# Kernel optimization log

Measured on AMD Instinct MI355X. Metric: run time of the kernel, lower is better.

The kernel has to match this reference:

```python
import jax, jax.numpy as jnp
import numpy as np

NUM_HEADS = 32
NUM_KV_HEADS = 8
HEAD_DIM = 128
SEQ = 2048
MASK_BLOCK = 128  # diffusion-LM denoising block size


def setup_inputs() -> dict:
    key = jax.random.key(0)
    kq, kk, kv = jax.random.split(key, 3)
    q = jax.random.normal(kq, (SEQ, NUM_HEADS * HEAD_DIM), dtype=jnp.float32)
    k = jax.random.normal(kk, (SEQ, NUM_KV_HEADS * HEAD_DIM), dtype=jnp.float32)
    v = jax.random.normal(kv, (SEQ, NUM_KV_HEADS * HEAD_DIM), dtype=jnp.float32)
    # block-causal mask at MASK_BLOCK granularity: token_q attends to token_kv
    # iff block(token_kv) <= block(token_q). Every row has >=1 True entry.
    blk = jnp.arange(SEQ) // MASK_BLOCK
    block_mask = blk[None, :] <= blk[:, None]  # [S, S] bool
    return {"q": q, "k": k, "v": v, "block_mask": block_mask}


def reference(q, k, v, block_mask):
    S = q.shape[0]
    scale = 1.0 / np.sqrt(HEAD_DIM).astype(np.float32)  # flex_attention default scale
    qh = q.reshape(S, NUM_HEADS, HEAD_DIM)       # [S, Hq, D]
    kh = k.reshape(S, NUM_KV_HEADS, HEAD_DIM)    # [S, Hkv, D]
    vh = v.reshape(S, NUM_KV_HEADS, HEAD_DIM)
    # GQA: repeat each kv head over its query-head group
    group = NUM_HEADS // NUM_KV_HEADS
    kh = jnp.repeat(kh, group, axis=1)           # [S, Hq, D]
    vh = jnp.repeat(vh, group, axis=1)
    scores = jnp.einsum('qhd,khd->hqk', qh, kh) * scale  # [Hq, S, S]
    neg_inf = jnp.finfo(scores.dtype).min
    scores = jnp.where(block_mask[None, :, :], scores, neg_inf)
    probs = jax.nn.softmax(scores, axis=-1)
    o = jnp.einsum('hqk,khd->qhd', probs, vh)    # [S, Hq, D]
    return o.reshape(S, NUM_HEADS * HEAD_DIM)
```

## Files before the change

kernel.cpp:

```cpp
#include <hip/hip_runtime.h>
#include <hip/hip_bf16.h>

#define SEQL  2048
#define NHQ   32
#define NHKV  8
#define HD    128

typedef __attribute__((ext_vector_type(4))) float          f32x4;
typedef __attribute__((ext_vector_type(8))) short          bf16x8;
typedef __attribute__((ext_vector_type(4))) unsigned short u16x4;
typedef __attribute__((ext_vector_type(8))) unsigned short u16x8;

__device__ __forceinline__ unsigned short f2bf(float f) {
  union { float f; unsigned u; } v; v.f = f;
  unsigned u = v.u;
  return (unsigned short)((u + 0x7fffu + ((u >> 16) & 1u)) >> 16);
}

__device__ __forceinline__ unsigned cvtpk_bf16(float lo, float hi) {
  unsigned r;
  asm("v_cvt_pk_bf16_f32 %0, %1, %2" : "=v"(r) : "v"(lo), "v"(hi));
  return r;
}

__device__ __forceinline__ void gload16(const void* g, void* l) {
  __builtin_amdgcn_global_load_lds(
      (const __attribute__((address_space(1))) unsigned int*)g,
      (__attribute__((address_space(3))) unsigned int*)l, 16, 0, 0);
}

__global__ __launch_bounds__(256) void prep_k(const float* __restrict__ k,
                                              unsigned short* __restrict__ kws) {
  int t = blockIdx.x * 256 + threadIdx.x;
  int s   = t >> 7;
  int col = (t & 127) << 3;
  int hkv = col >> 7;
  int d0  = col & 127;
  const float* src = k + (size_t)s * (NHKV * HD) + col;
  f32x4 a = *(const f32x4*)src;
  f32x4 b = *(const f32x4*)(src + 4);
  u16x8 r;
  r[0] = f2bf(a[0]); r[1] = f2bf(a[1]); r[2] = f2bf(a[2]); r[3] = f2bf(a[3]);
  r[4] = f2bf(b[0]); r[5] = f2bf(b[1]); r[6] = f2bf(b[2]); r[7] = f2bf(b[3]);
  int tile = s >> 6, rr = s & 63;
  int idx = (rr * 128 + d0) ^ ((rr & 7) << 3);
  *(u16x8*)(kws + (((size_t)(hkv * 32 + tile)) << 13) + idx) = r;
}

__global__ __launch_bounds__(256) void prep_v(const float* __restrict__ v,
                                              unsigned short* __restrict__ vws) {
  int t = blockIdx.x * 256 + threadIdx.x;
  int d    = t & 127;
  int hkv  = (t >> 7) & 7;
  int rest = t >> 10;
  int tile = rest >> 3;
  int g    = (rest >> 2) & 1;
  int lhi  = rest & 3;
  int s0   = tile * 64 + g * 32 + lhi * 4;
  const float* src = v + (size_t)s0 * (NHKV * HD) + hkv * HD + d;
  u16x8 r;
  #pragma unroll
  for (int j = 0; j < 8; ++j) {
    int soff = ((j >> 2) << 4) + (j & 3);
    r[j] = f2bf(src[(size_t)soff * (NHKV * HD)]);
  }
  int idx = (d * 64 + g * 32 + lhi * 8) ^ ((d & 7) << 3);
  *(u16x8*)(vws + (((size_t)(hkv * 32 + tile)) << 13) + idx) = r;
}

__global__ __launch_bounds__(256, 2) void attn_fwd11(
    const float* __restrict__ q,
    const unsigned short* __restrict__ kws,
    const unsigned short* __restrict__ vws,
    float* __restrict__ out)
{
  __shared__ unsigned short Kb[2][8192];
  __shared__ unsigned short Vb[2][8192];

  const int tid  = threadIdx.x;
  const int lane = tid & 63;
  const int wv   = tid >> 6;
  const int l15  = lane & 15;
  const int lhi  = lane >> 4;
  const int swzK = (l15 & 7) << 3;

  const int bx   = blockIdx.x;
  const int hkv  = bx & 7;
  const int h    = hkv * 4 + ((bx >> 3) & 3);
  const int pr   = bx >> 5;
  const int qtA  = pr, qtB = 31 - pr;
  const int nA   = ((qtA >> 1) + 1) * 2;
  const int T    = 34;

  const float qscale = 0.08838834764831845f * 1.4426950408889634f;
  const float THR = 11.5f;

  const unsigned short* ktiles = kws + (((size_t)hkv * 32) << 13);
  const unsigned short* vtiles = vws + (((size_t)hkv * 32) << 13);

  bf16x8 qf[4];
  f32x4 oacc[8];
  float mrun, lrun;

  auto loadQ = [&](int qt) {
    const float* qbase = q + (size_t)(qt * 64 + wv * 16 + l15) * (NHQ * HD) + h * HD + lhi * 8;
    #pragma unroll
    for (int c = 0; c < 4; ++c) {
      f32x4 a = *(const f32x4*)(qbase + c * 32);
      f32x4 b = *(const f32x4*)(qbase + c * 32 + 4);
      bf16x8 r;
      r[0] = (short)f2bf(a[0] * qscale);
      r[1] = (short)f2bf(a[1] * qscale);
      r[2] = (short)f2bf(a[2] * qscale);
      r[3] = (short)f2bf(a[3] * qscale);
      r[4] = (short)f2bf(b[0] * qscale);
      r[5] = (short)f2bf(b[1] * qscale);
      r[6] = (short)f2bf(b[2] * qscale);
      r[7] = (short)f2bf(b[3] * qscale);
      qf[c] = r;
    }
  };

  auto resetAcc = [&]() {
    #pragma unroll
    for (int i = 0; i < 8; ++i) oacc[i] = (f32x4){0.f, 0.f, 0.f, 0.f};
    mrun = -1e30f; lrun = 0.f;
  };

  auto epilogue = [&](int qt) {
    float invl = 1.0f / lrun;
    float* ob = out + (size_t)(qt * 64 + wv * 16 + l15) * (NHQ * HD) + h * HD + lhi * 4;
    #pragma unroll
    for (int dsub = 0; dsub < 8; ++dsub)
      *(f32x4*)(ob + dsub * 16) = oacc[dsub] * invl;
  };

  auto STAGE = [&](int b, int kvt) {
    const char* gk = (const char*)(ktiles + ((size_t)kvt << 13));
    const char* gv = (const char*)(vtiles + ((size_t)kvt << 13));
    char* lk = (char*)&Kb[b][0];
    char* lv = (char*)&Vb[b][0];
    #pragma unroll
    for (int i = 0; i < 4; ++i) {
      const int off = wv * 4096 + i * 1024;
      gload16(gk + off + lane * 16, lk + off);
      gload16(gv + off + lane * 16, lv + off);
    }
  };

  auto compute = [&](int b) {
    f32x4 sa[4];
    __builtin_amdgcn_s_setprio(1);
    #pragma unroll
    for (int sub = 0; sub < 4; ++sub) {
      f32x4 acc = (f32x4){0.f, 0.f, 0.f, 0.f};
      const int row = sub * 16 + l15;
      #pragma unroll
      for (int c = 0; c < 4; ++c) {
        bf16x8 kf = *(const bf16x8*)(&Kb[b][(row * 128 + c * 32 + lhi * 8) ^ swzK]);
        acc = __builtin_amdgcn_mfma_f32_16x16x32_bf16(kf, qf[c], acc, 0, 0, 0);
      }
      sa[sub] = acc;
    }
    __builtin_amdgcn_s_setprio(0);
    bf16x8 vr[2][8];
    #pragma unroll
    for (int kc = 0; kc < 2; ++kc)
      #pragma unroll
      for (int dsub = 0; dsub < 8; ++dsub) {
        const int d = dsub * 16 + l15;
        vr[kc][dsub] = *(const bf16x8*)(&Vb[b][(d * 64 + kc * 32 + lhi * 8) ^ swzK]);
      }
    float m0 = fmaxf(fmaxf(sa[0][0], sa[0][1]), fmaxf(sa[0][2], sa[0][3]));
    float m1 = fmaxf(fmaxf(sa[1][0], sa[1][1]), fmaxf(sa[1][2], sa[1][3]));
    float m2 = fmaxf(fmaxf(sa[2][0], sa[2][1]), fmaxf(sa[2][2], sa[2][3]));
    float m3 = fmaxf(fmaxf(sa[3][0], sa[3][1]), fmaxf(sa[3][2], sa[3][3]));
    float mt = fmaxf(fmaxf(m0, m1), fmaxf(m2, m3));
    mt = fmaxf(mt, __shfl_xor(mt, 16));
    mt = fmaxf(mt, __shfl_xor(mt, 32));
    if (__any(mt > mrun + THR)) {
      float mn = fmaxf(mrun, mt);
      float c0 = exp2f(mrun - mn);
      mrun = mn; lrun *= c0;
      #pragma unroll
      for (int d = 0; d < 8; ++d) oacc[d] *= c0;
    }
    unsigned pw[8];
    {
      float ts = 0.f;
      #pragma unroll
      for (int sub = 0; sub < 4; ++sub) {
        float p0 = exp2f(sa[sub][0] - mrun);
        float p1 = exp2f(sa[sub][1] - mrun);
        float p2 = exp2f(sa[sub][2] - mrun);
        float p3 = exp2f(sa[sub][3] - mrun);
        ts += (p0 + p1) + (p2 + p3);
        pw[2 * sub]     = cvtpk_bf16(p0, p1);
        pw[2 * sub + 1] = cvtpk_bf16(p2, p3);
      }
      ts += __shfl_xor(ts, 16);
      ts += __shfl_xor(ts, 32);
      lrun += ts;
    }
    __builtin_amdgcn_s_setprio(1);
    #pragma unroll
    for (int kc = 0; kc < 2; ++kc) {
      union { unsigned u[4]; bf16x8 v8; } pk;
      pk.u[0] = pw[4 * kc + 0];
      pk.u[1] = pw[4 * kc + 1];
      pk.u[2] = pw[4 * kc + 2];
      pk.u[3] = pw[4 * kc + 3];
      bf16x8 pf = pk.v8;
      #pragma unroll
      for (int dsub = 0; dsub < 8; ++dsub) {
        oacc[dsub] = __builtin_amdgcn_mfma_f32_16x16x32_bf16(vr[kc][dsub], pf, oacc[dsub], 0, 0, 0);
      }
    }
    __builtin_amdgcn_s_setprio(0);
  };

  loadQ(qtA);
  resetAcc();
  STAGE(0, 0);
  int buf = 0;
  for (int t = 0; t < T; ++t) {
    if (t == nA) { epilogue(qtA); loadQ(qtB); resetAcc(); }
    if (t + 1 < T) {
      const int p = t + 1;
      STAGE(buf ^ 1, (p < nA) ? p : p - nA);
      asm volatile("s_waitcnt vmcnt(8)" ::: "memory");
    } else {
      asm volatile("s_waitcnt vmcnt(0)" ::: "memory");
    }
    __builtin_amdgcn_s_barrier();
    asm volatile("" ::: "memory");
    compute(buf);
    asm volatile("" ::: "memory");
    __builtin_amdgcn_s_barrier();
    buf ^= 1;
  }
  epilogue(qtB);
}

__global__ __launch_bounds__(256) void attn_v1(
    const float* __restrict__ q,
    const float* __restrict__ k,
    const float* __restrict__ v,
    float* __restrict__ out)
{
  __shared__ unsigned short Ks[64 * 128];
  __shared__ unsigned short Vt[128 * 64];
  __shared__ unsigned short Psl[4][16 * 64];

  const int tid  = threadIdx.x;
  const int lane = tid & 63;
  const int wv   = tid >> 6;
  const int bx   = blockIdx.x;
  const int h    = bx & 31;
  const int qt   = (SEQL / 64 - 1) - (bx >> 5);
  const int q0   = qt * 64;
  const int hkv  = h >> 2;
  const int l15 = lane & 15;
  const int lhi = lane >> 4;
  const float qscale = 0.08838834764831845f * 1.4426950408889634f;

  bf16x8 qf[4];
  {
    const float* qbase = q + (size_t)(q0 + wv * 16 + l15) * (NHQ * HD) + h * HD + lhi * 8;
    #pragma unroll
    for (int c = 0; c < 4; ++c) {
      const float* p8 = qbase + c * 32;
      f32x4 a = *(const f32x4*)p8;
      f32x4 b = *(const f32x4*)(p8 + 4);
      bf16x8 r;
      r[0] = (short)f2bf(a[0] * qscale); r[1] = (short)f2bf(a[1] * qscale);
      r[2] = (short)f2bf(a[2] * qscale); r[3] = (short)f2bf(a[3] * qscale);
      r[4] = (short)f2bf(b[0] * qscale); r[5] = (short)f2bf(b[1] * qscale);
      r[6] = (short)f2bf(b[2] * qscale); r[7] = (short)f2bf(b[3] * qscale);
      qf[c] = r;
    }
  }
  f32x4 oacc[8];
  #pragma unroll
  for (int i = 0; i < 8; ++i) oacc[i] = (f32x4){0.f, 0.f, 0.f, 0.f};
  float mrun[4], lrun[4];
  #pragma unroll
  for (int r = 0; r < 4; ++r) { mrun[r] = -1e30f; lrun[r] = 0.f; }
  const int ntiles = ((q0 >> 7) + 1) * 2;
  for (int t = 0; t < ntiles; ++t) {
    const int kv0 = t * 64;
    __syncthreads();
    #pragma unroll
    for (int it = 0; it < 8; ++it) {
      int c = it * 256 + tid;
      int row = c >> 5;
      int dc = (c & 31) << 2;
      f32x4 x = *(const f32x4*)(k + (size_t)(kv0 + row) * (NHKV * HD) + hkv * HD + dc);
      u16x4 y;
      y[0] = f2bf(x[0]); y[1] = f2bf(x[1]); y[2] = f2bf(x[2]); y[3] = f2bf(x[3]);
      int idx = (row * HD + dc) ^ ((row & 7) << 3);
      *(u16x4*)(&Ks[idx]) = y;
    }
    {
      int row = tid >> 2;
      int db = (tid & 3) << 5;
      const float* vbase = v + (size_t)(kv0 + row) * (NHKV * HD) + hkv * HD + db;
      #pragma unroll
      for (int it = 0; it < 8; ++it) {
        f32x4 x = *(const f32x4*)(vbase + it * 4);
        int d0 = db + it * 4;
        #pragma unroll
        for (int j = 0; j < 4; ++j) {
          int d = d0 + j;
          int idx = (d * 64 + row) ^ ((d & 7) << 3);
          Vt[idx] = f2bf(x[j]);
        }
      }
    }
    __syncthreads();
    f32x4 sacc[4];
    #pragma unroll
    for (int sub = 0; sub < 4; ++sub) {
      f32x4 acc = (f32x4){0.f, 0.f, 0.f, 0.f};
      #pragma unroll
      for (int c = 0; c < 4; ++c) {
        int row = sub * 16 + l15;
        int idx = (row * HD + c * 32 + lhi * 8) ^ ((row & 7) << 3);
        bf16x8 kf = *(const bf16x8*)(&Ks[idx]);
        acc = __builtin_amdgcn_mfma_f32_16x16x32_bf16(qf[c], kf, acc, 0, 0, 0);
      }
      sacc[sub] = acc;
    }
    float corr[4];
    #pragma unroll
    for (int r = 0; r < 4; ++r) {
      float mt = fmaxf(fmaxf(sacc[0][r], sacc[1][r]), fmaxf(sacc[2][r], sacc[3][r]));
      #pragma unroll
      for (int off = 1; off < 16; off <<= 1) mt = fmaxf(mt, __shfl_xor(mt, off));
      float mnew = fmaxf(mrun[r], mt);
      corr[r] = exp2f(mrun[r] - mnew);
      mrun[r] = mnew;
      float p0 = exp2f(sacc[0][r] - mnew);
      float p1 = exp2f(sacc[1][r] - mnew);
      float p2 = exp2f(sacc[2][r] - mnew);
      float p3 = exp2f(sacc[3][r] - mnew);
      int qr = (lhi << 2) + r;
      int swz = (qr & 7) << 3;
      int bq = qr * 64;
      Psl[wv][(bq + 0  + l15) ^ swz] = f2bf(p0);
      Psl[wv][(bq + 16 + l15) ^ swz] = f2bf(p1);
      Psl[wv][(bq + 32 + l15) ^ swz] = f2bf(p2);
      Psl[wv][(bq + 48 + l15) ^ swz] = f2bf(p3);
      float ts = p0 + p1 + p2 + p3;
      #pragma unroll
      for (int off = 1; off < 16; off <<= 1) ts += __shfl_xor(ts, off);
      lrun[r] = lrun[r] * corr[r] + ts;
    }
    #pragma unroll
    for (int dsub = 0; dsub < 8; ++dsub) {
      f32x4 o = oacc[dsub];
      o[0] *= corr[0]; o[1] *= corr[1]; o[2] *= corr[2]; o[3] *= corr[3];
      oacc[dsub] = o;
    }
    #pragma unroll
    for (int kc = 0; kc < 2; ++kc) {
      int pidx = (l15 * 64 + kc * 32 + lhi * 8) ^ ((l15 & 7) << 3);
      bf16x8 pf = *(const bf16x8*)(&Psl[wv][pidx]);
      #pragma unroll
      for (int dsub = 0; dsub < 8; ++dsub) {
        int d = dsub * 16 + l15;
        int vidx = (d * 64 + kc * 32 + lhi * 8) ^ ((d & 7) << 3);
        bf16x8 vf = *(const bf16x8*)(&Vt[vidx]);
        oacc[dsub] = __builtin_amdgcn_mfma_f32_16x16x32_bf16(pf, vf, oacc[dsub], 0, 0, 0);
      }
    }
  }
  float inv[4];
  #pragma unroll
  for (int r = 0; r < 4; ++r) inv[r] = 1.0f / lrun[r];
  float* obase = out + (size_t)(q0 + wv * 16 + (lhi << 2)) * (NHQ * HD) + h * HD + l15;
  #pragma unroll
  for (int dsub = 0; dsub < 8; ++dsub) {
    #pragma unroll
    for (int r = 0; r < 4; ++r) {
      obase[(size_t)r * (NHQ * HD) + dsub * 16] = oacc[dsub][r] * inv[r];
    }
  }
}

extern "C" void kernel_launch(void* const* d_in, const int* in_sizes, int n_in,
                              void* d_out, int out_size, void* d_ws, size_t ws_size,
                              hipStream_t stream) {
  const float* q = (const float*)d_in[0];
  const float* k = (const float*)d_in[1];
  const float* v = (const float*)d_in[2];
  float* out = (float*)d_out;
  const size_t prepNeed = (size_t)8 * 1024 * 1024 + 512;
  if (ws_size >= prepNeed) {
    unsigned short* kws = (unsigned short*)d_ws;
    unsigned short* vws = kws + (size_t)4 * 1024 * 1024 / 2;
    prep_k<<<1024, 256, 0, stream>>>(k, kws);
    prep_v<<<1024, 256, 0, stream>>>(v, vws);
    attn_fwd11<<<512, 256, 0, stream>>>(q, kws, vws, out);
  } else {
    attn_v1<<<1024, 256, 0, stream>>>(q, k, v, out);
  }
}
```

Before: 85.56 us.

## Share K/V tiles between paired query tiles in a dual-accumulator loop

Each block now processes both paired query tiles (qtA, qtB) together over the shared KV prefix. Every staged K/V tile feeds two sets of MFMAs, one per query tile, so the shared prefix is loaded once instead of twice. The block then finishes qtB alone. This roughly halves K/V LDS and global traffic for the shared part, at the cost of twice the accumulator and Q-fragment registers, which risks spills or lower occupancy under launch_bounds(256,2). The block-to-pair mapping is also permuted to balance per-block work, since trip counts now differ between blocks (nB = 34 - nA).

```diff
diff --git a/kernel.cpp b/kernel.cpp
--- a/kernel.cpp
+++ b/kernel.cpp
@@ -68,7 +68,7 @@
   *(u16x8*)(vws + (((size_t)(hkv * 32 + tile)) << 13) + idx) = r;
 }
 
-__global__ __launch_bounds__(256, 2) void attn_fwd11(
+__global__ __launch_bounds__(256, 2) void attn_fwd12(
     const float* __restrict__ q,
     const unsigned short* __restrict__ kws,
     const unsigned short* __restrict__ vws,
@@ -87,10 +87,11 @@
   const int bx   = blockIdx.x;
   const int hkv  = bx & 7;
   const int h    = hkv * 4 + ((bx >> 3) & 3);
-  const int pr   = bx >> 5;
+  const int idx2 = bx >> 5;
+  const int pr   = (idx2 < 8) ? idx2 : (23 - idx2);
   const int qtA  = pr, qtB = 31 - pr;
   const int nA   = ((qtA >> 1) + 1) * 2;
-  const int T    = 34;
+  const int nB   = 34 - nA;
 
   const float qscale = 0.08838834764831845f * 1.4426950408889634f;
   const float THR = 11.5f;
@@ -98,12 +99,12 @@
   const unsigned short* ktiles = kws + (((size_t)hkv * 32) << 13);
   const unsigned short* vtiles = vws + (((size_t)hkv * 32) << 13);
 
-  bf16x8 qf[4];
-  f32x4 oacc[8];
-  float mrun, lrun;
-
-  auto loadQ = [&](int qt) {
-    const float* qbase = q + (size_t)(qt * 64 + wv * 16 + l15) * (NHQ * HD) + h * HD + lhi * 8;
+  bf16x8 qfA[4], qfB[4];
+  f32x4 oaccA[8], oaccB[8];
+  float mrunA = -1e30f, lrunA = 0.f, mrunB = -1e30f, lrunB = 0.f;
+
+  {
+    const float* qbase = q + (size_t)(qtA * 64 + wv * 16 + l15) * (NHQ * HD) + h * HD + lhi * 8;
     #pragma unroll
     for (int c = 0; c < 4; ++c) {
       f32x4 a = *(const f32x4*)(qbase + c * 32);
@@ -117,23 +118,32 @@
       r[5] = (short)f2bf(b[1] * qscale);
       r[6] = (short)f2bf(b[2] * qscale);
       r[7] = (short)f2bf(b[3] * qscale);
-      qf[c] = r;
-    }
-  };
-
-  auto resetAcc = [&]() {
-    #pragma unroll
-    for (int i = 0; i < 8; ++i) oacc[i] = (f32x4){0.f, 0.f, 0.f, 0.f};
-    mrun = -1e30f; lrun = 0.f;
-  };
-
-  auto epilogue = [&](int qt) {
-    float invl = 1.0f / lrun;
-    float* ob = out + (size_t)(qt * 64 + wv * 16 + l15) * (NHQ * HD) + h * HD + lhi * 4;
-    #pragma unroll
-    for (int dsub = 0; dsub < 8; ++dsub)
-      *(f32x4*)(ob + dsub * 16) = oacc[dsub] * invl;
-  };
+      qfA[c] = r;
+    }
+  }
+  {
+    const float* qbase = q + (size_t)(qtB * 64 + wv * 16 + l15) * (NHQ * HD) + h * HD + lhi * 8;
+    #pragma unroll
+    for (int c = 0; c < 4; ++c) {
+      f32x4 a = *(const f32x4*)(qbase + c * 32);
+      f32x4 b = *(const f32x4*)(qbase + c * 32 + 4);
+      bf16x8 r;
+      r[0] = (short)f2bf(a[0] * qscale);
+      r[1] = (short)f2bf(a[1] * qscale);
+      r[2] = (short)f2bf(a[2] * qscale);
+      r[3] = (short)f2bf(a[3] * qscale);
+      r[4] = (short)f2bf(b[0] * qscale);
+      r[5] = (short)f2bf(b[1] * qscale);
+      r[6] = (short)f2bf(b[2] * qscale);
+      r[7] = (short)f2bf(b[3] * qscale);
+      qfB[c] = r;
+    }
+  }
+  #pragma unroll
+  for (int i = 0; i < 8; ++i) {
+    oaccA[i] = (f32x4){0.f, 0.f, 0.f, 0.f};
+    oaccB[i] = (f32x4){0.f, 0.f, 0.f, 0.f};
+  }
 
   auto STAGE = [&](int b, int kvt) {
     const char* gk = (const char*)(ktiles + ((size_t)kvt << 13));
@@ -148,7 +158,104 @@
     }
   };
 
-  auto compute = [&](int b) {
+  auto computeDual = [&](int b) {
+    f32x4 saA[4], saB[4];
+    __builtin_amdgcn_s_setprio(1);
+    #pragma unroll
+    for (int sub = 0; sub < 4; ++sub) {
+      f32x4 aA = (f32x4){0.f, 0.f, 0.f, 0.f};
+      f32x4 aB = (f32x4){0.f, 0.f, 0.f, 0.f};
+      const int row = sub * 16 + l15;
+      #pragma unroll
+      for (int c = 0; c < 4; ++c) {
+        bf16x8 kf = *(const bf16x8*)(&Kb[b][(row * 128 + c * 32 + lhi * 8) ^ swzK]);
+        aA = __builtin_amdgcn_mfma_f32_16x16x32_bf16(kf, qfA[c], aA, 0, 0, 0);
+        aB = __builtin_amdgcn_mfma_f32_16x16x32_bf16(kf, qfB[c], aB, 0, 0, 0);
+      }
+      saA[sub] = aA; saB[sub] = aB;
+    }
+    __builtin_amdgcn_s_setprio(0);
+    float a0 = fmaxf(fmaxf(saA[0][0], saA[0][1]), fmaxf(saA[0][2], saA[0][3]));
+    float a1 = fmaxf(fmaxf(saA[1][0], saA[1][1]), fmaxf(saA[1][2], saA[1][3]));
+    float a2 = fmaxf(fmaxf(saA[2][0], saA[2][1]), fmaxf(saA[2][2], saA[2][3]));
+    float a3 = fmaxf(fmaxf(saA[3][0], saA[3][1]), fmaxf(saA[3][2], saA[3][3]));
+    float mtA = fmaxf(fmaxf(a0, a1), fmaxf(a2, a3));
+    float b0 = fmaxf(fmaxf(saB[0][0], saB[0][1]), fmaxf(saB[0][2], saB[0][3]));
+    float b1 = fmaxf(fmaxf(saB[1][0], saB[1][1]), fmaxf(saB[1][2], saB[1][3]));
+    float b2 = fmaxf(fmaxf(saB[2][0], saB[2][1]), fmaxf(saB[2][2], saB[2][3]));
+    float b3 = fmaxf(fmaxf(saB[3][0], saB[3][1]), fmaxf(saB[3][2], saB[3][3]));
+    float mtB = fmaxf(fmaxf(b0, b1), fmaxf(b2, b3));
+    mtA = fmaxf(mtA, __shfl_xor(mtA, 16));
+    mtA = fmaxf(mtA, __shfl_xor(mtA, 32));
+    mtB = fmaxf(mtB, __shfl_xor(mtB, 16));
+    mtB = fmaxf(mtB, __shfl_xor(mtB, 32));
+    int need = (mtA > mrunA + THR) || (mtB > mrunB + THR);
+    if (__any(need)) {
+      float mnA = fmaxf(mrunA, mtA), mnB = fmaxf(mrunB, mtB);
+      float cA = exp2f(mrunA - mnA), cB = exp2f(mrunB - mnB);
+      mrunA = mnA; mrunB = mnB;
+      lrunA *= cA; lrunB *= cB;
+      #pragma unroll
+      for (int d = 0; d < 8; ++d) { oaccA[d] *= cA; oaccB[d] *= cB; }
+    }
+    unsigned pwA[8], pwB[8];
+    {
+      float ts = 0.f;
+      #pragma unroll
+      for (int sub = 0; sub < 4; ++sub) {
+        float p0 = exp2f(saA[sub][0] - mrunA);
+        float p1 = exp2f(saA[sub][1] - mrunA);
+        float p2 = exp2f(saA[sub][2] - mrunA);
+        float p3 = exp2f(saA[sub][3] - mrunA);
+        ts += (p0 + p1) + (p2 + p3);
+        pwA[2 * sub]     = cvtpk_bf16(p0, p1);
+        pwA[2 * sub + 1] = cvtpk_bf16(p2, p3);
+      }
+      ts += __shfl_xor(ts, 16);
+      ts += __shfl_xor(ts, 32);
+      lrunA += ts;
+    }
+    {
+      float ts = 0.f;
+      #pragma unroll
+      for (int sub = 0; sub < 4; ++sub) {
+        float p0 = exp2f(saB[sub][0] - mrunB);
+        float p1 = exp2f(saB[sub][1] - mrunB);
+        float p2 = exp2f(saB[sub][2] - mrunB);
+        float p3 = exp2f(saB[sub][3] - mrunB);
+        ts += (p0 + p1) + (p2 + p3);
+        pwB[2 * sub]     = cvtpk_bf16(p0, p1);
+        pwB[2 * sub + 1] = cvtpk_bf16(p2, p3);
+      }
+      ts += __shfl_xor(ts, 16);
+      ts += __shfl_xor(ts, 32);
+      lrunB += ts;
+    }
+    __builtin_amdgcn_s_setprio(1);
+    #pragma unroll
+    for (int kc = 0; kc < 2; ++kc) {
+      bf16x8 vr[8];
+      #pragma unroll
+      for (int dsub = 0; dsub < 8; ++dsub) {
+        const int d = dsub * 16 + l15;
+        vr[dsub] = *(const bf16x8*)(&Vb[b][(d * 64 + kc * 32 + lhi * 8) ^ swzK]);
+      }
+      union { unsigned u[4]; bf16x8 v8; } pA, pB;
+      pA.u[0] = pwA[4 * kc + 0]; pA.u[1] = pwA[4 * kc + 1];
+      pA.u[2] = pwA[4 * kc + 2]; pA.u[3] = pwA[4 * kc + 3];
+      pB.u[0] = pwB[4 * kc + 0]; pB.u[1] = pwB[4 * kc + 1];
+      pB.u[2] = pwB[4 * kc + 2]; pB.u[3] = pwB[4 * kc + 3];
+      bf16x8 pfA = pA.v8, pfB = pB.v8;
+      #pragma unroll
+      for (int dsub = 0; dsub < 8; ++dsub) {
+        oaccA[dsub] = __builtin_amdgcn_mfma_f32_16x16x32_bf16(vr[dsub], pfA, oaccA[dsub], 0, 0, 0);
+        oaccB[dsub] = __builtin_amdgcn_mfma_f32_16x16x32_bf16(vr[dsub], pfB, oaccB[dsub], 0, 0, 0);
+      }
+    }
+    __builtin_amdgcn_s_setprio(0);
+  };
+
+  auto computeB = [&](int b) {
     f32x4 sa[4];
     __builtin_amdgcn_s_setprio(1);
     #pragma unroll
@@ -158,7 +265,7 @@
       #pragma unroll
       for (int c = 0; c < 4; ++c) {
         bf16x8 kf = *(const bf16x8*)(&Kb[b][(row * 128 + c * 32 + lhi * 8) ^ swzK]);
-        acc = __builtin_amdgcn_mfma_f32_16x16x32_bf16(kf, qf[c], acc, 0, 0, 0);
+        acc = __builtin_amdgcn_mfma_f32_16x16x32_bf16(kf, qfB[c], acc, 0, 0, 0);
       }
       sa[sub] = acc;
     }
@@ -178,29 +285,29 @@
     float mt = fmaxf(fmaxf(m0, m1), fmaxf(m2, m3));
     mt = fmaxf(mt, __shfl_xor(mt, 16));
     mt = fmaxf(mt, __shfl_xor(mt, 32));
-    if (__any(mt > mrun + THR)) {
-      float mn = fmaxf(mrun, mt);
-      float c0 = exp2f(mrun - mn);
-      mrun = mn; lrun *= c0;
-      #pragma unroll
-      for (int d = 0; d < 8; ++d) oacc[d] *= c0;
+    if (__any(mt > mrunB + THR)) {
+      float mn = fmaxf(mrunB, mt);
+      float c0 = exp2f(mrunB - mn);
+      mrunB = mn; lrunB *= c0;
+      #pragma unroll
+      for (int d = 0; d < 8; ++d) oaccB[d] *= c0;
     }
     unsigned pw[8];
     {
       float ts = 0.f;
       #pragma unroll
       for (int sub = 0; sub < 4; ++sub) {
-        float p0 = exp2f(sa[sub][0] - mrun);
-        float p1 = exp2f(sa[sub][1] - mrun);
-        float p2 = exp2f(sa[sub][2] - mrun);
-        float p3 = exp2f(sa[sub][3] - mrun);
+        float p0 = exp2f(sa[sub][0] - mrunB);
+        float p1 = exp2f(sa[sub][1] - mrunB);
+        float p2 = exp2f(sa[sub][2] - mrunB);
+        float p3 = exp2f(sa[sub][3] - mrunB);
         ts += (p0 + p1) + (p2 + p3);
         pw[2 * sub]     = cvtpk_bf16(p0, p1);
         pw[2 * sub + 1] = cvtpk_bf16(p2, p3);
       }
       ts += __shfl_xor(ts, 16);
       ts += __shfl_xor(ts, 32);
-      lrun += ts;
+      lrunB += ts;
     }
     __builtin_amdgcn_s_setprio(1);
     #pragma unroll
@@ -213,33 +320,44 @@
       bf16x8 pf = pk.v8;
       #pragma unroll
       for (int dsub = 0; dsub < 8; ++dsub) {
-        oacc[dsub] = __builtin_amdgcn_mfma_f32_16x16x32_bf16(vr[kc][dsub], pf, oacc[dsub], 0, 0, 0);
+        oaccB[dsub] = __builtin_amdgcn_mfma_f32_16x16x32_bf16(vr[kc][dsub], pf, oaccB[dsub], 0, 0, 0);
       }
     }
     __builtin_amdgcn_s_setprio(0);
   };
 
-  loadQ(qtA);
-  resetAcc();
   STAGE(0, 0);
   int buf = 0;
-  for (int t = 0; t < T; ++t) {
-    if (t == nA) { epilogue(qtA); loadQ(qtB); resetAcc(); }
-    if (t + 1 < T) {
-      const int p = t + 1;
-      STAGE(buf ^ 1, (p < nA) ? p : p - nA);
+  #pragma unroll 1
+  for (int t = 0; t < nB; ++t) {
+    if (t == nA) {
+      float invl = 1.0f / lrunA;
+      float* ob = out + (size_t)(qtA * 64 + wv * 16 + l15) * (NHQ * HD) + h * HD + lhi * 4;
+      #pragma unroll
+      for (int dsub = 0; dsub < 8; ++dsub)
+        *(f32x4*)(ob + dsub * 16) = oaccA[dsub] * invl;
+    }
+    if (t + 1 < nB) {
+      STAGE(buf ^ 1, t + 1);
       asm volatile("s_waitcnt vmcnt(8)" ::: "memory");
     } else {
       asm volatile("s_waitcnt vmcnt(0)" ::: "memory");
     }
     __builtin_amdgcn_s_barrier();
     asm volatile("" ::: "memory");
-    compute(buf);
+    if (t < nA) computeDual(buf);
+    else        computeB(buf);
     asm volatile("" ::: "memory");
     __builtin_amdgcn_s_barrier();
     buf ^= 1;
   }
-  epilogue(qtB);
+  {
+    float invl = 1.0f / lrunB;
+    float* ob = out + (size_t)(qtB * 64 + wv * 16 + l15) * (NHQ * HD) + h * HD + lhi * 4;
+    #pragma unroll
+    for (int dsub = 0; dsub < 8; ++dsub)
+      *(f32x4*)(ob + dsub * 16) = oaccB[dsub] * invl;
+  }
 }
 
 __global__ __launch_bounds__(256) void attn_v1(
@@ -401,7 +519,7 @@
     unsigned short* vws = kws + (size_t)4 * 1024 * 1024 / 2;
     prep_k<<<1024, 256, 0, stream>>>(k, kws);
     prep_v<<<1024, 256, 0, stream>>>(v, vws);
-    attn_fwd11<<<512, 256, 0, stream>>>(q, kws, vws, out);
+    attn_fwd12<<<512, 256, 0, stream>>>(q, kws, vws, out);
   } else {
     attn_v1<<<1024, 256, 0, stream>>>(q, k, v, out);
   }
```

Result: slower. 101.5 us (+18.7%).

## Switch attention kernel to 32x32x16 MFMA with two waves of 32 query rows

Applied to the files above, without the earlier changes.

Rewrites the attention kernel to use 32x32x16 bf16 MFMA instead of 16x16x32. Each block now has 2 waves, each owning 32 query rows, and the V workspace layout is reordered to match the new operand fragment. Larger MFMA tiles reduce LDS fragment reads per FLOP and remove one cross-lane shuffle in the softmax reductions. In exchange, the smaller 128-thread blocks mean each wave stages more data. Register pressure also rises from the 16-wide accumulators, which may cut occupancy.

```diff
diff --git a/kernel.cpp b/kernel.cpp
--- a/kernel.cpp
+++ b/kernel.cpp
@@ -6,10 +6,11 @@
 #define NHKV  8
 #define HD    128
 
-typedef __attribute__((ext_vector_type(4))) float          f32x4;
-typedef __attribute__((ext_vector_type(8))) short          bf16x8;
-typedef __attribute__((ext_vector_type(4))) unsigned short u16x4;
-typedef __attribute__((ext_vector_type(8))) unsigned short u16x8;
+typedef __attribute__((ext_vector_type(4)))  float          f32x4;
+typedef __attribute__((ext_vector_type(16))) float          f32x16;
+typedef __attribute__((ext_vector_type(8)))  short          bf16x8;
+typedef __attribute__((ext_vector_type(4)))  unsigned short u16x4;
+typedef __attribute__((ext_vector_type(8)))  unsigned short u16x8;
 
 __device__ __forceinline__ unsigned short f2bf(float f) {
   union { float f; unsigned u; } v; v.f = f;
@@ -54,21 +55,21 @@
   int hkv  = (t >> 7) & 7;
   int rest = t >> 10;
   int tile = rest >> 3;
-  int g    = (rest >> 2) & 1;
-  int lhi  = rest & 3;
-  int s0   = tile * 64 + g * 32 + lhi * 4;
+  int s    = (rest >> 1) & 3;
+  int hh   = rest & 1;
+  int s0   = tile * 64 + s * 16 + hh * 4;
   const float* src = v + (size_t)s0 * (NHKV * HD) + hkv * HD + d;
   u16x8 r;
   #pragma unroll
   for (int j = 0; j < 8; ++j) {
-    int soff = ((j >> 2) << 4) + (j & 3);
+    int soff = ((j >> 2) << 3) + (j & 3);
     r[j] = f2bf(src[(size_t)soff * (NHKV * HD)]);
   }
-  int idx = (d * 64 + g * 32 + lhi * 8) ^ ((d & 7) << 3);
+  int idx = (d * 64 + s * 16 + hh * 8) ^ ((d & 7) << 3);
   *(u16x8*)(vws + (((size_t)(hkv * 32 + tile)) << 13) + idx) = r;
 }
 
-__global__ __launch_bounds__(256, 2) void attn_fwd11(
+__global__ __launch_bounds__(128) void attn_fwd14(
     const float* __restrict__ q,
     const unsigned short* __restrict__ kws,
     const unsigned short* __restrict__ vws,
@@ -80,9 +81,8 @@
   const int tid  = threadIdx.x;
   const int lane = tid & 63;
   const int wv   = tid >> 6;
-  const int l15  = lane & 15;
-  const int lhi  = lane >> 4;
-  const int swzK = (l15 & 7) << 3;
+  const int l31  = lane & 31;
+  const int h8   = lane >> 5;
 
   const int bx   = blockIdx.x;
   const int hkv  = bx & 7;
@@ -98,16 +98,16 @@
   const unsigned short* ktiles = kws + (((size_t)hkv * 32) << 13);
   const unsigned short* vtiles = vws + (((size_t)hkv * 32) << 13);
 
-  bf16x8 qf[4];
-  f32x4 oacc[8];
+  bf16x8 qf[8];
+  f32x16 oacc[4];
   float mrun, lrun;
 
   auto loadQ = [&](int qt) {
-    const float* qbase = q + (size_t)(qt * 64 + wv * 16 + l15) * (NHQ * HD) + h * HD + lhi * 8;
-    #pragma unroll
-    for (int c = 0; c < 4; ++c) {
-      f32x4 a = *(const f32x4*)(qbase + c * 32);
-      f32x4 b = *(const f32x4*)(qbase + c * 32 + 4);
+    const float* qbase = q + (size_t)(qt * 64 + wv * 32 + l31) * (NHQ * HD) + h * HD + h8 * 8;
+    #pragma unroll
+    for (int c = 0; c < 8; ++c) {
+      f32x4 a = *(const f32x4*)(qbase + c * 16);
+      f32x4 b = *(const f32x4*)(qbase + c * 16 + 4);
       bf16x8 r;
       r[0] = (short)f2bf(a[0] * qscale);
       r[1] = (short)f2bf(a[1] * qscale);
@@ -123,16 +123,26 @@
 
   auto resetAcc = [&]() {
     #pragma unroll
-    for (int i = 0; i < 8; ++i) oacc[i] = (f32x4){0.f, 0.f, 0.f, 0.f};
+    for (int i = 0; i < 4; ++i)
+      oacc[i] = (f32x16){0.f,0.f,0.f,0.f,0.f,0.f,0.f,0.f,0.f,0.f,0.f,0.f,0.f,0.f,0.f,0.f};
     mrun = -1e30f; lrun = 0.f;
   };
 
   auto epilogue = [&](int qt) {
     float invl = 1.0f / lrun;
-    float* ob = out + (size_t)(qt * 64 + wv * 16 + l15) * (NHQ * HD) + h * HD + lhi * 4;
-    #pragma unroll
-    for (int dsub = 0; dsub < 8; ++dsub)
-      *(f32x4*)(ob + dsub * 16) = oacc[dsub] * invl;
+    float* ob = out + (size_t)(qt * 64 + wv * 32 + l31) * (NHQ * HD) + h * HD + h8 * 4;
+    #pragma unroll
+    for (int db = 0; db < 4; ++db) {
+      #pragma unroll
+      for (int rq = 0; rq < 4; ++rq) {
+        f32x4 vv;
+        vv[0] = oacc[db][4 * rq + 0] * invl;
+        vv[1] = oacc[db][4 * rq + 1] * invl;
+        vv[2] = oacc[db][4 * rq + 2] * invl;
+        vv[3] = oacc[db][4 * rq + 3] * invl;
+        *(f32x4*)(ob + db * 32 + rq * 8) = vv;
+      }
+    }
   };
 
   auto STAGE = [&](int b, int kvt) {
@@ -141,80 +151,79 @@
     char* lk = (char*)&Kb[b][0];
     char* lv = (char*)&Vb[b][0];
     #pragma unroll
-    for (int i = 0; i < 4; ++i) {
-      const int off = wv * 4096 + i * 1024;
+    for (int i = 0; i < 8; ++i) {
+      const int off = wv * 8192 + i * 1024;
       gload16(gk + off + lane * 16, lk + off);
       gload16(gv + off + lane * 16, lv + off);
     }
   };
 
   auto compute = [&](int b) {
-    f32x4 sa[4];
+    f32x16 s0 = (f32x16){0.f,0.f,0.f,0.f,0.f,0.f,0.f,0.f,0.f,0.f,0.f,0.f,0.f,0.f,0.f,0.f};
+    f32x16 s1 = s0;
     __builtin_amdgcn_s_setprio(1);
     #pragma unroll
-    for (int sub = 0; sub < 4; ++sub) {
-      f32x4 acc = (f32x4){0.f, 0.f, 0.f, 0.f};
-      const int row = sub * 16 + l15;
-      #pragma unroll
-      for (int c = 0; c < 4; ++c) {
-        bf16x8 kf = *(const bf16x8*)(&Kb[b][(row * 128 + c * 32 + lhi * 8) ^ swzK]);
-        acc = __builtin_amdgcn_mfma_f32_16x16x32_bf16(kf, qf[c], acc, 0, 0, 0);
-      }
-      sa[sub] = acc;
+    for (int c = 0; c < 8; ++c) {
+      const int r0 = l31;
+      const int r1 = 32 + l31;
+      bf16x8 kf0 = *(const bf16x8*)(&Kb[b][(r0 * 128 + c * 16 + h8 * 8) ^ ((r0 & 7) << 3)]);
+      bf16x8 kf1 = *(const bf16x8*)(&Kb[b][(r1 * 128 + c * 16 + h8 * 8) ^ ((r1 & 7) << 3)]);
+      s0 = __builtin_amdgcn_mfma_f32_32x32x16_bf16(kf0, qf[c], s0, 0, 0, 0);
+      s1 = __builtin_amdgcn_mfma_f32_32x32x16_bf16(kf1, qf[c], s1, 0, 0, 0);
     }
     __builtin_amdgcn_s_setprio(0);
-    bf16x8 vr[2][8];
-    #pragma unroll
-    for (int kc = 0; kc < 2; ++kc)
-      #pragma unroll
-      for (int dsub = 0; dsub < 8; ++dsub) {
-        const int d = dsub * 16 + l15;
-        vr[kc][dsub] = *(const bf16x8*)(&Vb[b][(d * 64 + kc * 32 + lhi * 8) ^ swzK]);
-      }
-    float m0 = fmaxf(fmaxf(sa[0][0], sa[0][1]), fmaxf(sa[0][2], sa[0][3]));
-    float m1 = fmaxf(fmaxf(sa[1][0], sa[1][1]), fmaxf(sa[1][2], sa[1][3]));
-    float m2 = fmaxf(fmaxf(sa[2][0], sa[2][1]), fmaxf(sa[2][2], sa[2][3]));
-    float m3 = fmaxf(fmaxf(sa[3][0], sa[3][1]), fmaxf(sa[3][2], sa[3][3]));
-    float mt = fmaxf(fmaxf(m0, m1), fmaxf(m2, m3));
-    mt = fmaxf(mt, __shfl_xor(mt, 16));
+    float m0 = fmaxf(fmaxf(s0[0], s0[1]),  fmaxf(s0[2], s0[3]));
+    float m1 = fmaxf(fmaxf(s0[4], s0[5]),  fmaxf(s0[6], s0[7]));
+    float m2 = fmaxf(fmaxf(s0[8], s0[9]),  fmaxf(s0[10], s0[11]));
+    float m3 = fmaxf(fmaxf(s0[12], s0[13]), fmaxf(s0[14], s0[15]));
+    float m4 = fmaxf(fmaxf(s1[0], s1[1]),  fmaxf(s1[2], s1[3]));
+    float m5 = fmaxf(fmaxf(s1[4], s1[5]),  fmaxf(s1[6], s1[7]));
+    float m6 = fmaxf(fmaxf(s1[8], s1[9]),  fmaxf(s1[10], s1[11]));
+    float m7 = fmaxf(fmaxf(s1[12], s1[13]), fmaxf(s1[14], s1[15]));
+    float mt = fmaxf(fmaxf(fmaxf(m0, m1), fmaxf(m2, m3)),
+                     fmaxf(fmaxf(m4, m5), fmaxf(m6, m7)));
     mt = fmaxf(mt, __shfl_xor(mt, 32));
     if (__any(mt > mrun + THR)) {
       float mn = fmaxf(mrun, mt);
       float c0 = exp2f(mrun - mn);
       mrun = mn; lrun *= c0;
       #pragma unroll
-      for (int d = 0; d < 8; ++d) oacc[d] *= c0;
-    }
-    unsigned pw[8];
-    {
-      float ts = 0.f;
-      #pragma unroll
-      for (int sub = 0; sub < 4; ++sub) {
-        float p0 = exp2f(sa[sub][0] - mrun);
-        float p1 = exp2f(sa[sub][1] - mrun);
-        float p2 = exp2f(sa[sub][2] - mrun);
-        float p3 = exp2f(sa[sub][3] - mrun);
-        ts += (p0 + p1) + (p2 + p3);
-        pw[2 * sub]     = cvtpk_bf16(p0, p1);
-        pw[2 * sub + 1] = cvtpk_bf16(p2, p3);
+      for (int i = 0; i < 4; ++i) oacc[i] *= c0;
+    }
+    unsigned pw[16];
+    float ts = 0.f;
+    #pragma unroll
+    for (int i = 0; i < 8; ++i) {
+      float p0 = exp2f(s0[2 * i]     - mrun);
+      float p1 = exp2f(s0[2 * i + 1] - mrun);
+      ts += p0 + p1;
+      pw[i] = cvtpk_bf16(p0, p1);
+    }
+    #pragma unroll
+    for (int i = 0; i < 8; ++i) {
+      float p0 = exp2f(s1[2 * i]     - mrun);
+      float p1 = exp2f(s1[2 * i + 1] - mrun);
+      ts += p0 + p1;
+      pw[8 + i] = cvtpk_bf16(p0, p1);
+    }
+    ts += __shfl_xor(ts, 32);
+    lrun += ts;
+    __builtin_amdgcn_s_setprio(1);
+    #pragma unroll
+    for (int db = 0; db < 4; ++db) {
+      const int d = db * 32 + l31;
+      f32x16 acc = oacc[db];
+      #pragma unroll
+      for (int s = 0; s < 4; ++s) {
+        bf16x8 vf = *(const bf16x8*)(&Vb[b][(d * 64 + s * 16 + h8 * 8) ^ ((d & 7) << 3)]);
+        union { unsigned u[4]; bf16x8 v8; } pk;
+        pk.u[0] = pw[4 * s + 0];
+        pk.u[1] = pw[4 * s + 1];
+        pk.u[2] = pw[4 * s + 2];
+        pk.u[3] = pw[4 * s + 3];
+        acc = __builtin_amdgcn_mfma_f32_32x32x16_bf16(vf, pk.v8, acc, 0, 0, 0);
       }
-      ts += __shfl_xor(ts, 16);
-      ts += __shfl_xor(ts, 32);
-      lrun += ts;
-    }
-    __builtin_amdgcn_s_setprio(1);
-    #pragma unroll
-    for (int kc = 0; kc < 2; ++kc) {
-      union { unsigned u[4]; bf16x8 v8; } pk;
-      pk.u[0] = pw[4 * kc + 0];
-      pk.u[1] = pw[4 * kc + 1];
-      pk.u[2] = pw[4 * kc + 2];
-      pk.u[3] = pw[4 * kc + 3];
-      bf16x8 pf = pk.v8;
-      #pragma unroll
-      for (int dsub = 0; dsub < 8; ++dsub) {
-        oacc[dsub] = __builtin_amdgcn_mfma_f32_16x16x32_bf16(vr[kc][dsub], pf, oacc[dsub], 0, 0, 0);
-      }
+      oacc[db] = acc;
     }
     __builtin_amdgcn_s_setprio(0);
   };
@@ -223,12 +232,13 @@
   resetAcc();
   STAGE(0, 0);
   int buf = 0;
+  #pragma unroll 1
   for (int t = 0; t < T; ++t) {
     if (t == nA) { epilogue(qtA); loadQ(qtB); resetAcc(); }
     if (t + 1 < T) {
       const int p = t + 1;
       STAGE(buf ^ 1, (p < nA) ? p : p - nA);
-      asm volatile("s_waitcnt vmcnt(8)" ::: "memory");
+      asm volatile("s_waitcnt vmcnt(16)" ::: "memory");
     } else {
       asm volatile("s_waitcnt vmcnt(0)" ::: "memory");
     }
@@ -401,7 +411,7 @@
     unsigned short* vws = kws + (size_t)4 * 1024 * 1024 / 2;
     prep_k<<<1024, 256, 0, stream>>>(k, kws);
     prep_v<<<1024, 256, 0, stream>>>(v, vws);
-    attn_fwd11<<<512, 256, 0, stream>>>(q, kws, vws, out);
+    attn_fwd14<<<512, 128, 0, stream>>>(q, kws, vws, out);
   } else {
     attn_v1<<<1024, 256, 0, stream>>>(q, k, v, out);
   }
```

After: 97.51 us. +14.0%, slower.
